# Performance work log

Measured on AMD Instinct MI355X. Metric: run time of the kernel, lower is better.

The kernel has to match this reference:

```python
import jax, jax.numpy as jnp
import numpy as np

N = 10000
E = 320000
D_IN = 256
D_OUT = 256
EPS = 0.2  # initial value of trainable eps


def setup_inputs() -> dict:
    key = jax.random.key(0)
    ks = jax.random.split(key, 7)
    x = jax.random.normal(ks[0], (N, D_IN), dtype=jnp.float32)
    edge_index = jax.random.randint(ks[1], (2, E), 0, N, dtype=jnp.int64)
    # MLP params (Linear(in,out) -> ReLU -> Linear(out,out)), Kaiming-ish scale
    w1 = jax.random.normal(ks[2], (D_IN, D_OUT), dtype=jnp.float32) / np.sqrt(D_IN)
    b1 = jnp.zeros((D_OUT,), dtype=jnp.float32)
    w2 = jax.random.normal(ks[3], (D_OUT, D_OUT), dtype=jnp.float32) / np.sqrt(D_OUT)
    b2 = jnp.zeros((D_OUT,), dtype=jnp.float32)
    eps = jnp.float32(EPS)
    return {"x": x, "edge_index": edge_index, "w1": w1, "b1": b1,
            "w2": w2, "b2": b2, "eps": eps}


def reference(x, edge_index, w1, b1, w2, b2, eps):
    src, dst = edge_index[0], edge_index[1]
    # GIN sum aggregation: agg[i] = sum_{(j->i) in E} x[j]
    msgs = x[src]  # [E, D_IN] gather
    agg = jax.ops.segment_sum(msgs, dst, num_segments=N)  # [N, D_IN] scatter-add
    h = (1.0 + eps) * x + agg
    # 2-layer MLP
    h = jax.nn.relu(h @ w1 + b1)
    out = h @ w2 + b2
    return out
```

## Files before the change

### kernel.cpp

```cpp
#include <hip/hip_runtime.h>

#define NN 10000
#define NE 320000
#define RCAP 64
#define BSTRIDE 128

typedef __bf16 bf16x8 __attribute__((ext_vector_type(8)));
typedef float f32x4 __attribute__((ext_vector_type(4)));
typedef unsigned short us8 __attribute__((ext_vector_type(8)));

static __device__ __forceinline__ unsigned short f2bf(float f) {
  union { float fv; unsigned u; } v; v.fv = f;
  unsigned r = v.u + 0x7FFFu + ((v.u >> 16) & 1u);
  return (unsigned short)(r >> 16);
}
static __device__ __forceinline__ float bf2f(unsigned short b) {
  union { unsigned u; float f; } v; v.u = ((unsigned)b) << 16;
  return v.f;
}


__global__ __launch_bounds__(256) void conv_k(const float* __restrict__ x,
                                              const float* __restrict__ w1,
                                              const float* __restrict__ w2,
                                              ushort4* __restrict__ xb4,
                                              unsigned short* __restrict__ w1t,
                                              unsigned short* __restrict__ w2t,
                                              int* __restrict__ cnt) {
  __shared__ unsigned short sh[64][72];
  int bid = blockIdx.x, tid = threadIdx.x;
  if (bid < 2500) {
    int t = bid * 256 + tid;
    if (t < 20480) cnt[t] = 0;
    float4 v = reinterpret_cast<const float4*>(x)[t];
    ushort4 o;
    o.x = f2bf(v.x); o.y = f2bf(v.y); o.z = f2bf(v.z); o.w = f2bf(v.w);
    xb4[t] = o;
  } else {
    int b2 = bid - 2500;
    const float* w = (b2 & 16) ? w2 : w1;
    unsigned short* wt = (b2 & 16) ? w2t : w1t;
    int tile = b2 & 15;
    int ki0 = (tile >> 2) * 64, ni0 = (tile & 3) * 64;
    int r = tid >> 4, c = tid & 15;
#pragma unroll
    for (int rr = r; rr < 64; rr += 16) {
      float4 v = *reinterpret_cast<const float4*>(&w[(ki0 + rr) * 256 + ni0 + c * 4]);
      ushort4 o;
      o.x = f2bf(v.x); o.y = f2bf(v.y); o.z = f2bf(v.z); o.w = f2bf(v.w);
      *reinterpret_cast<ushort4*>(&sh[rr][c * 4]) = o;
    }
    __syncthreads();
    int n = tid >> 3, c8 = tid & 7;
#pragma unroll
    for (int nn = n; nn < 64; nn += 32) {
      us8 o;
#pragma unroll
      for (int j = 0; j < 8; ++j) o[j] = sh[c8 * 8 + j][nn];
      *reinterpret_cast<us8*>(&wt[(ni0 + nn) * 256 + ki0 + c8 * 8]) = o;
    }
  }
}


__global__ __launch_bounds__(256) void fill_k(const int* __restrict__ ei,
                                              int* __restrict__ cnt,
                                              int* __restrict__ bucket) {
  int e = (blockIdx.x * 256 + threadIdx.x) * 4;
  if (e < NE) {
    int4 s = *reinterpret_cast<const int4*>(&ei[e]);
    int4 d = *reinterpret_cast<const int4*>(&ei[NE + e]);
    int p;
    p = atomicAdd(&cnt[d.x], 1);
    if (p < RCAP) bucket[d.x * BSTRIDE + p] = s.x;
    p = atomicAdd(&cnt[10240 + d.y], 1);
    if (p < RCAP) bucket[d.y * BSTRIDE + RCAP + p] = s.y;
    p = atomicAdd(&cnt[d.z], 1);
    if (p < RCAP) bucket[d.z * BSTRIDE + p] = s.z;
    p = atomicAdd(&cnt[10240 + d.w], 1);
    if (p < RCAP) bucket[d.w * BSTRIDE + RCAP + p] = s.w;
  }
}


__global__ __launch_bounds__(256) void agg_k(const us8* __restrict__ xb8,
                                             const int* __restrict__ cnt,
                                             const int* __restrict__ bucket,
                                             const float* __restrict__ epsp,
                                             unsigned short* __restrict__ hb) {
  __shared__ float part[2][256];
  int tid = threadIdx.x;
  int wave = tid >> 6;
  int slot = wave >> 1;
  int p = wave & 1;
  int node = blockIdx.x * 2 + slot;
  int lane = tid & 63;
  int half = lane >> 5, off = lane & 31;
  float e1 = 1.0f + epsp[0];

  float a[8];
  if (p == 0) {
    us8 sv = xb8[node * 32 + off];
    float selfw = half ? 0.0f : e1;
#pragma unroll
    for (int j = 0; j < 8; ++j) a[j] = bf2f(sv[j]) * selfw;
  } else {
#pragma unroll
    for (int j = 0; j < 8; ++j) a[j] = 0.0f;
  }

  int m = min(cnt[p * 10240 + node], RCAP);
  const int4* bp4 = reinterpret_cast<const int4*>(bucket + node * BSTRIDE + p * RCAP);
  int4 ia = bp4[0], ib = bp4[1];
  int k = 0;
  while (k + 8 <= m) {
    int4 na = bp4[(k >> 2) + 2];
    int4 nb = bp4[(k >> 2) + 3];
    int r0 = half ? ia.y : ia.x;
    int r1 = half ? ia.w : ia.z;
    int r2 = half ? ib.y : ib.x;
    int r3 = half ? ib.w : ib.z;
    us8 v0 = xb8[r0 * 32 + off];
    us8 v1 = xb8[r1 * 32 + off];
    us8 v2 = xb8[r2 * 32 + off];
    us8 v3 = xb8[r3 * 32 + off];
#pragma unroll
    for (int j = 0; j < 8; ++j)
      a[j] += (bf2f(v0[j]) + bf2f(v1[j])) + (bf2f(v2[j]) + bf2f(v3[j]));
    ia = na; ib = nb; k += 8;
  }
  int tl = m - k;
#pragma unroll
  for (int q = 0; q < 4; ++q) {
    int idx = (q == 0) ? (half ? ia.y : ia.x)
            : (q == 1) ? (half ? ia.w : ia.z)
            : (q == 2) ? (half ? ib.y : ib.x)
                       : (half ? ib.w : ib.z);
    if (2 * q + half < tl) {
      us8 v = xb8[idx * 32 + off];
#pragma unroll
      for (int j = 0; j < 8; ++j) a[j] += bf2f(v[j]);
    }
  }
#pragma unroll
  for (int j = 0; j < 8; ++j) a[j] += __shfl_xor(a[j], 32);
  if (p == 1 && half == 0) {
#pragma unroll
    for (int j = 0; j < 8; ++j) part[slot][j * 32 + off] = a[j];
  }
  __syncthreads();
  if (p == 0 && half == 0) {
    us8 o;
#pragma unroll
    for (int j = 0; j < 8; ++j) o[j] = f2bf(a[j] + part[slot][j * 32 + off]);
    *reinterpret_cast<us8*>(&hb[node * 256 + off * 8]) = o;
  }
}


__global__ __launch_bounds__(256) void mlp_k(const unsigned short* __restrict__ hb,
                                             const unsigned short* __restrict__ w1t,
                                             const float* __restrict__ b1,
                                             const unsigned short* __restrict__ w2t,
                                             const float* __restrict__ b2,
                                             float* __restrict__ out) {
  __shared__ unsigned short As[32][264];
  __shared__ unsigned short Bs[256][72];
  int m0 = blockIdx.x * 32;
  int tid = threadIdx.x;
  int lane = tid & 63, wave = tid >> 6;
  int waveM = wave & 1, waveN = wave >> 1;
  int l15 = lane & 15, g = lane >> 4;
#pragma unroll
  for (int i = 0; i < 4; ++i) {
    int c = tid + i * 256;
    int r = c >> 5, cc = c & 31;
    int4 v = (m0 + r < NN)
                 ? *reinterpret_cast<const int4*>(&hb[(m0 + r) * 256 + cc * 8])
                 : make_int4(0, 0, 0, 0);
    *reinterpret_cast<int4*>(&As[r][cc * 8]) = v;
  }
  float bias1[8], bias2[8];
#pragma unroll
  for (int ni = 0; ni < 8; ++ni) {
    int col = waveN * 128 + ni * 16 + l15;
    bias1[ni] = b1[col];
    bias2[ni] = b2[col];
  }
  f32x4 acc[8];
#pragma unroll
  for (int ni = 0; ni < 8; ++ni) acc[ni] = f32x4{0.f, 0.f, 0.f, 0.f};
  for (int k0 = 0; k0 < 256; k0 += 64) {
#pragma unroll
    for (int i = 0; i < 8; ++i) {
      int c = tid + i * 256;
      int n = c >> 3, kc = c & 7;
      *reinterpret_cast<int4*>(&Bs[n][kc * 8]) =
          *reinterpret_cast<const int4*>(&w1t[n * 256 + k0 + kc * 8]);
    }
    __syncthreads();
#pragma unroll
    for (int kk = 0; kk < 2; ++kk) {
      bf16x8 af = *reinterpret_cast<const bf16x8*>(
          &As[waveM * 16 + l15][k0 + kk * 32 + g * 8]);
#pragma unroll
      for (int ni = 0; ni < 8; ++ni) {
        bf16x8 bfr = *reinterpret_cast<const bf16x8*>(
            &Bs[waveN * 128 + ni * 16 + l15][kk * 32 + g * 8]);
        acc[ni] = __builtin_amdgcn_mfma_f32_16x16x32_bf16(af, bfr, acc[ni], 0, 0, 0);
      }
    }
    __syncthreads();
  }
#pragma unroll
  for (int ni = 0; ni < 8; ++ni) {
    int col = waveN * 128 + ni * 16 + l15;
#pragma unroll
    for (int r = 0; r < 4; ++r) {
      int row = waveM * 16 + g * 4 + r;
      As[row][col] = f2bf(fmaxf(acc[ni][r] + bias1[ni], 0.f));
    }
    acc[ni] = f32x4{0.f, 0.f, 0.f, 0.f};
  }
  for (int k0 = 0; k0 < 256; k0 += 64) {
#pragma unroll
    for (int i = 0; i < 8; ++i) {
      int c = tid + i * 256;
      int n = c >> 3, kc = c & 7;
      *reinterpret_cast<int4*>(&Bs[n][kc * 8]) =
          *reinterpret_cast<const int4*>(&w2t[n * 256 + k0 + kc * 8]);
    }
    __syncthreads();
#pragma unroll
    for (int kk = 0; kk < 2; ++kk) {
      bf16x8 af = *reinterpret_cast<const bf16x8*>(
          &As[waveM * 16 + l15][k0 + kk * 32 + g * 8]);
#pragma unroll
      for (int ni = 0; ni < 8; ++ni) {
        bf16x8 bfr = *reinterpret_cast<const bf16x8*>(
            &Bs[waveN * 128 + ni * 16 + l15][kk * 32 + g * 8]);
        acc[ni] = __builtin_amdgcn_mfma_f32_16x16x32_bf16(af, bfr, acc[ni], 0, 0, 0);
      }
    }
    __syncthreads();
  }
#pragma unroll
  for (int ni = 0; ni < 8; ++ni) {
    int col = waveN * 128 + ni * 16 + l15;
#pragma unroll
    for (int r = 0; r < 4; ++r) {
      int row = m0 + waveM * 16 + g * 4 + r;
      if (row < NN) out[row * 256 + col] = acc[ni][r] + bias2[ni];
    }
  }
}


extern "C" void kernel_launch(void* const* d_in, const int* in_sizes, int n_in,
                              void* d_out, int out_size, void* d_ws, size_t ws_size,
                              hipStream_t stream) {
  const float* x = (const float*)d_in[0];
  const int* ei = (const int*)d_in[1];
  const float* w1 = (const float*)d_in[2];
  const float* b1 = (const float*)d_in[3];
  const float* w2 = (const float*)d_in[4];
  const float* b2 = (const float*)d_in[5];
  const float* eps = (const float*)d_in[6];
  float* out = (float*)d_out;

  int* cnt = (int*)d_ws;
  int* bucket = cnt + 20480;
  unsigned short* xb = (unsigned short*)(bucket + NN * BSTRIDE + 32);
  unsigned short* w1t = xb + NN * 256;
  unsigned short* w2t = w1t + 65536;
  unsigned short* hb = w2t + 65536;

  conv_k<<<2532, 256, 0, stream>>>(x, w1, w2, (ushort4*)xb, w1t, w2t, cnt);
  fill_k<<<(NE / 4 + 255) / 256, 256, 0, stream>>>(ei, cnt, bucket);
  agg_k<<<NN / 2, 256, 0, stream>>>((const us8*)xb, cnt, bucket, eps, hb);
  mlp_k<<<(NN + 31) / 32, 256, 0, stream>>>(hb, w1t, b1, w2t, b2, out);
}
```

Measured before the change: 60.42 us.

## Enlarge MLP tile to 64 rows with 8 waves and 2x4 MFMA tiles

The fused two-layer MLP kernel now processes 64 rows per block with 512 threads instead of 32 rows with 256. Each wave computes a 32x64 output tile (2x4 MFMA fragments) instead of 16x128. The aim is to halve the per-row reloading of the weight tiles into shared memory and to reuse each B fragment across two A fragments. In exchange the grid drops from about 313 to 157 blocks, which may underfill the 256 CUs, and per-block LDS use grows.

New measurement: 59.73 us. About the same (-1.2%).

```diff
diff --git a/kernel.cpp b/kernel.cpp
--- a/kernel.cpp
+++ b/kernel.cpp
@@ -158,42 +158,46 @@
 }
 
 
-__global__ __launch_bounds__(256) void mlp_k(const unsigned short* __restrict__ hb,
+__global__ __launch_bounds__(512) void mlp_k(const unsigned short* __restrict__ hb,
                                              const unsigned short* __restrict__ w1t,
                                              const float* __restrict__ b1,
                                              const unsigned short* __restrict__ w2t,
                                              const float* __restrict__ b2,
                                              float* __restrict__ out) {
-  __shared__ unsigned short As[32][264];
+  __shared__ unsigned short As[64][264];
   __shared__ unsigned short Bs[256][72];
-  int m0 = blockIdx.x * 32;
+  int m0 = blockIdx.x * 64;
   int tid = threadIdx.x;
   int lane = tid & 63, wave = tid >> 6;
   int waveM = wave & 1, waveN = wave >> 1;
   int l15 = lane & 15, g = lane >> 4;
+
 #pragma unroll
   for (int i = 0; i < 4; ++i) {
-    int c = tid + i * 256;
+    int c = tid + i * 512;
     int r = c >> 5, cc = c & 31;
     int4 v = (m0 + r < NN)
                  ? *reinterpret_cast<const int4*>(&hb[(m0 + r) * 256 + cc * 8])
                  : make_int4(0, 0, 0, 0);
     *reinterpret_cast<int4*>(&As[r][cc * 8]) = v;
   }
-  float bias1[8], bias2[8];
-#pragma unroll
-  for (int ni = 0; ni < 8; ++ni) {
-    int col = waveN * 128 + ni * 16 + l15;
+  float bias1[4], bias2[4];
+#pragma unroll
+  for (int ni = 0; ni < 4; ++ni) {
+    int col = waveN * 64 + ni * 16 + l15;
     bias1[ni] = b1[col];
     bias2[ni] = b2[col];
   }
-  f32x4 acc[8];
-#pragma unroll
-  for (int ni = 0; ni < 8; ++ni) acc[ni] = f32x4{0.f, 0.f, 0.f, 0.f};
+  f32x4 acc[2][4];
+#pragma unroll
+  for (int mi = 0; mi < 2; ++mi)
+#pragma unroll
+    for (int ni = 0; ni < 4; ++ni) acc[mi][ni] = f32x4{0.f, 0.f, 0.f, 0.f};
+
   for (int k0 = 0; k0 < 256; k0 += 64) {
 #pragma unroll
-    for (int i = 0; i < 8; ++i) {
-      int c = tid + i * 256;
+    for (int i = 0; i < 4; ++i) {
+      int c = tid + i * 512;
       int n = c >> 3, kc = c & 7;
       *reinterpret_cast<int4*>(&Bs[n][kc * 8]) =
           *reinterpret_cast<const int4*>(&w1t[n * 256 + k0 + kc * 8]);
@@ -201,31 +205,38 @@
     __syncthreads();
 #pragma unroll
     for (int kk = 0; kk < 2; ++kk) {
-      bf16x8 af = *reinterpret_cast<const bf16x8*>(
-          &As[waveM * 16 + l15][k0 + kk * 32 + g * 8]);
-#pragma unroll
-      for (int ni = 0; ni < 8; ++ni) {
-        bf16x8 bfr = *reinterpret_cast<const bf16x8*>(
-            &Bs[waveN * 128 + ni * 16 + l15][kk * 32 + g * 8]);
-        acc[ni] = __builtin_amdgcn_mfma_f32_16x16x32_bf16(af, bfr, acc[ni], 0, 0, 0);
+#pragma unroll
+      for (int mi = 0; mi < 2; ++mi) {
+        bf16x8 af = *reinterpret_cast<const bf16x8*>(
+            &As[waveM * 32 + mi * 16 + l15][k0 + kk * 32 + g * 8]);
+#pragma unroll
+        for (int ni = 0; ni < 4; ++ni) {
+          bf16x8 bfr = *reinterpret_cast<const bf16x8*>(
+              &Bs[waveN * 64 + ni * 16 + l15][kk * 32 + g * 8]);
+          acc[mi][ni] =
+              __builtin_amdgcn_mfma_f32_16x16x32_bf16(af, bfr, acc[mi][ni], 0, 0, 0);
+        }
       }
     }
     __syncthreads();
   }
 #pragma unroll
-  for (int ni = 0; ni < 8; ++ni) {
-    int col = waveN * 128 + ni * 16 + l15;
-#pragma unroll
-    for (int r = 0; r < 4; ++r) {
-      int row = waveM * 16 + g * 4 + r;
-      As[row][col] = f2bf(fmaxf(acc[ni][r] + bias1[ni], 0.f));
-    }
-    acc[ni] = f32x4{0.f, 0.f, 0.f, 0.f};
+  for (int mi = 0; mi < 2; ++mi) {
+#pragma unroll
+    for (int ni = 0; ni < 4; ++ni) {
+      int col = waveN * 64 + ni * 16 + l15;
+#pragma unroll
+      for (int r = 0; r < 4; ++r) {
+        int row = waveM * 32 + mi * 16 + g * 4 + r;
+        As[row][col] = f2bf(fmaxf(acc[mi][ni][r] + bias1[ni], 0.f));
+      }
+      acc[mi][ni] = f32x4{0.f, 0.f, 0.f, 0.f};
+    }
   }
   for (int k0 = 0; k0 < 256; k0 += 64) {
 #pragma unroll
-    for (int i = 0; i < 8; ++i) {
-      int c = tid + i * 256;
+    for (int i = 0; i < 4; ++i) {
+      int c = tid + i * 512;
       int n = c >> 3, kc = c & 7;
       *reinterpret_cast<int4*>(&Bs[n][kc * 8]) =
           *reinterpret_cast<const int4*>(&w2t[n * 256 + k0 + kc * 8]);
@@ -233,24 +244,31 @@
     __syncthreads();
 #pragma unroll
     for (int kk = 0; kk < 2; ++kk) {
-      bf16x8 af = *reinterpret_cast<const bf16x8*>(
-          &As[waveM * 16 + l15][k0 + kk * 32 + g * 8]);
-#pragma unroll
-      for (int ni = 0; ni < 8; ++ni) {
-        bf16x8 bfr = *reinterpret_cast<const bf16x8*>(
-            &Bs[waveN * 128 + ni * 16 + l15][kk * 32 + g * 8]);
-        acc[ni] = __builtin_amdgcn_mfma_f32_16x16x32_bf16(af, bfr, acc[ni], 0, 0, 0);
+#pragma unroll
+      for (int mi = 0; mi < 2; ++mi) {
+        bf16x8 af = *reinterpret_cast<const bf16x8*>(
+            &As[waveM * 32 + mi * 16 + l15][k0 + kk * 32 + g * 8]);
+#pragma unroll
+        for (int ni = 0; ni < 4; ++ni) {
+          bf16x8 bfr = *reinterpret_cast<const bf16x8*>(
+              &Bs[waveN * 64 + ni * 16 + l15][kk * 32 + g * 8]);
+          acc[mi][ni] =
+              __builtin_amdgcn_mfma_f32_16x16x32_bf16(af, bfr, acc[mi][ni], 0, 0, 0);
+        }
       }
     }
     __syncthreads();
   }
 #pragma unroll
-  for (int ni = 0; ni < 8; ++ni) {
-    int col = waveN * 128 + ni * 16 + l15;
-#pragma unroll
-    for (int r = 0; r < 4; ++r) {
-      int row = m0 + waveM * 16 + g * 4 + r;
-      if (row < NN) out[row * 256 + col] = acc[ni][r] + bias2[ni];
+  for (int mi = 0; mi < 2; ++mi) {
+#pragma unroll
+    for (int ni = 0; ni < 4; ++ni) {
+      int col = waveN * 64 + ni * 16 + l15;
+#pragma unroll
+      for (int r = 0; r < 4; ++r) {
+        int row = m0 + waveM * 32 + mi * 16 + g * 4 + r;
+        if (row < NN) out[row * 256 + col] = acc[mi][ni][r] + bias2[ni];
+      }
     }
   }
 }
@@ -278,5 +296,5 @@
   conv_k<<<2532, 256, 0, stream>>>(x, w1, w2, (ushort4*)xb, w1t, w2t, cnt);
   fill_k<<<(NE / 4 + 255) / 256, 256, 0, stream>>>(ei, cnt, bucket);
   agg_k<<<NN / 2, 256, 0, stream>>>((const us8*)xb, cnt, bucket, eps, hb);
-  mlp_k<<<(NN + 31) / 32, 256, 0, stream>>>(hb, w1t, b1, w2t, b2, out);
-}
+  mlp_k<<<(NN + 63) / 64, 512, 0, stream>>>(hb, w1t, b1, w2t, b2, out);
+}
```
